# Kernel optimization log

Measured on AMD Instinct MI355X. Metric: run time of the kernel, lower is better.

Reference implementation:

```python
import jax, jax.numpy as jnp
import numpy as np

B, T, P = 4, 1000, 300
C, D, CC = 512, 256, 256
H, NL, FF = 8, 4, 2048
L = P + T
DH = C // H


def _sin_emb(t, dim):
    half = dim // 2
    freqs = jnp.exp(-jnp.arange(half, dtype=jnp.float32) * (np.log(10000.0) / (half - 1)))
    a = t[:, None].astype(jnp.float32) * freqs[None, :]
    return jnp.concatenate([jnp.sin(a), jnp.cos(a)], axis=-1)


def _pos_emb(pos, dim):
    # fairseq-style sinusoidal table evaluated at integer positions (padding_idx+1 offset already applied by caller)
    half = dim // 2
    freqs = jnp.exp(-jnp.arange(half, dtype=jnp.float32) * (np.log(10000.0) / (half - 1)))
    a = pos[..., None].astype(jnp.float32) * freqs
    return jnp.concatenate([jnp.sin(a), jnp.cos(a)], axis=-1)


def _ln(x, g, b, eps=1e-5):
    m = jnp.mean(x, -1, keepdims=True)
    v = jnp.mean((x - m) ** 2, -1, keepdims=True)
    return (x - m) * jax.lax.rsqrt(v + eps) * g + b


def _mish(x):
    return x * jnp.tanh(jax.nn.softplus(x))


def _mha(x, key_pad, Wqkv, bqkv, Wo, bo):
    qkv = x @ Wqkv + bqkv
    q, k, v = jnp.split(qkv, 3, axis=-1)
    q = q.reshape(B, L, H, DH)
    k = k.reshape(B, L, H, DH)
    v = v.reshape(B, L, H, DH)
    s = jnp.einsum('blhd,bmhd->bhlm', q, k) / np.sqrt(DH)
    s = jnp.where(key_pad[:, None, None, :], -1e9, s)  # mask padded keys
    a = jax.nn.softmax(s, axis=-1)
    o = jnp.einsum('bhlm,bmhd->blhd', a, v).reshape(B, L, C)
    return o @ Wo + bo


def _layer(x, key_pad, skip, p):
    Wqkv, bqkv, Wo, bo, g1, b1, g2, b2, W1, bf1, W2, bf2 = p
    if skip is not None:
        x = (x + skip) / np.sqrt(2.0)
    x = x + _mha(_ln(x, g1, b1), key_pad, Wqkv, bqkv, Wo, bo)
    attn_skip = x
    h = _ln(x, g2, b2)
    x = x + jax.nn.relu(h @ W1 + bf1) @ W2 + bf2
    return x, attn_skip, x


def _fwd(spec, diffusion_step, cond, prompt,
         spec_W, spec_b, cond_W, cond_b, prompt_W, prompt_b,
         mlp_W1, mlp_b1, mlp_W2, mlp_b2, out_W, out_b, skip_W, skip_b,
         Wqkv, bqkv, Wo, bo, ln1_g, ln1_b, ln2_g, ln2_b,
         ffn_W1, ffn_b1, ffn_W2, ffn_b2, x_mask, prompt_mask):
    spec_h = jnp.einsum('bdt,dc->btc', spec, spec_W) + spec_b      # [B,T,C]
    cond_h = jnp.einsum('bdt,dc->btc', cond, cond_W) + cond_b      # [B,T,C]
    prompt_h = prompt @ prompt_W + prompt_b                        # [B,P,C]

    def mlp(e):
        return _mish(e @ mlp_W1 + mlp_b1) @ mlp_W2 + mlp_b2

    dstep = mlp(_sin_emb(diffusion_step, D))                       # [B,C]
    pstep = mlp(_sin_emb(jnp.zeros((B,), jnp.float32), D))         # [B,C]

    pl = jnp.sum(~prompt_mask, axis=1)                              # prompt lengths
    sl = jnp.sum(~x_mask, axis=1)                                   # spec lengths
    j = jnp.arange(L)[None, :]
    plb, slb = pl[:, None], sl[:, None]
    in_prompt = j < plb
    in_spec = (j >= plb) & (j < plb + slb)

    pidx = jnp.clip(j, 0, P - 1)
    sidx = jnp.clip(j - plb, 0, T - 1)
    gp = jnp.take_along_axis(prompt_h, pidx[..., None], axis=1)
    gs = jnp.take_along_axis(spec_h, sidx[..., None], axis=1)
    packed = jnp.where(in_prompt[..., None], gp,
                       jnp.where(in_spec[..., None], gs, 0.0))      # [B,L,C]
    step_packed = jnp.where(in_prompt[..., None], pstep[:, None, :],
                            jnp.where(in_spec[..., None], dstep[:, None, :], 0.0))
    cond_packed = jnp.where(in_spec[..., None],
                            jnp.take_along_axis(cond_h, sidx[..., None], axis=1), 0.0)
    key_pad = ~(in_prompt | in_spec)                                # True = padding slot
    # positions restart at padding_idx+1=1 for each segment (prompt / spec / pad)
    pos = jnp.where(in_prompt, j + 1,
                    jnp.where(in_spec, j - plb + 1, j - plb - slb + 1))

    x = packed + _pos_emb(pos, C)
    # decoder: x = x + cond ; x = x + diffusion_step (dropout identity in eval)
    x = x + cond_packed + step_packed

    in_collect, ffn_skips = [], []
    for i in range(NL // 2):
        p = (Wqkv[i], bqkv[i], Wo[i], bo[i], ln1_g[i], ln1_b[i], ln2_g[i], ln2_b[i],
             ffn_W1[i], ffn_b1[i], ffn_W2[i], ffn_b2[i])
        x, _, f = _layer(x, key_pad, None, p)
        in_collect.append(x)
        ffn_skips.append(f)
    for i in range(NL // 2, NL):
        p = (Wqkv[i], bqkv[i], Wo[i], bo[i], ln1_g[i], ln1_b[i], ln2_g[i], ln2_b[i],
             ffn_W1[i], ffn_b1[i], ffn_W2[i], ffn_b2[i])
        x, _, f = _layer(x, key_pad, in_collect.pop(), p)
        ffn_skips.append(f)

    x = sum(ffn_skips) / np.sqrt(float(NL))
    x = jax.nn.relu(x @ skip_W + skip_b)
    x = x @ out_W + out_b                                           # [B,L,D]
    xidx = plb + jnp.arange(T)[None, :]                             # gather spec slots
    x = jnp.take_along_axis(x, xidx[..., None], axis=1)             # [B,T,D]
    return x.transpose(0, 2, 1)                                     # [B,D,T]


def setup_inputs() -> dict:
    key = jax.random.key(0)
    it = iter(jax.random.split(key, 40))
    def n(shape, s=0.02):
        return jax.random.normal(next(it), shape, jnp.float32) * s
    spec = jax.random.normal(next(it), (B, D, T), jnp.float32)
    cond = jax.random.normal(next(it), (B, CC, T), jnp.float32)
    prompt = jax.random.normal(next(it), (B, P, D), jnp.float32)
    diffusion_step = jax.random.uniform(next(it), (B,), jnp.float32) * 1000.0
    spec_len = jax.random.randint(next(it), (B,), T // 2, T + 1)
    prompt_len = jax.random.randint(next(it), (B,), P // 2, P + 1)
    x_mask = jnp.arange(T)[None, :] >= spec_len[:, None]
    prompt_mask = jnp.arange(P)[None, :] >= prompt_len[:, None]
    spk = jnp.zeros((B,), jnp.int32)
    return dict(
        spec=spec, x_mask=x_mask, diffusion_step=diffusion_step, cond=cond,
        spk=spk, prompt=prompt, prompt_mask=prompt_mask,
        spec_W=n((D, C)), spec_b=jnp.zeros((C,)),
        cond_W=n((CC, C)), cond_b=jnp.zeros((C,)),
        prompt_W=n((D, C)), prompt_b=jnp.zeros((C,)),
        mlp_W1=n((D, 4 * D)), mlp_b1=jnp.zeros((4 * D,)),
        mlp_W2=n((4 * D, C)), mlp_b2=jnp.zeros((C,)),
        out_W=n((C, D)), out_b=jnp.zeros((D,)),
        skip_W=n((C, C)), skip_b=jnp.zeros((C,)),
        Wqkv=n((NL, C, 3 * C)), bqkv=jnp.zeros((NL, 3 * C)),
        Wo=n((NL, C, C)), bo=jnp.zeros((NL, C)),
        ln1_g=jnp.ones((NL, C)), ln1_b=jnp.zeros((NL, C)),
        ln2_g=jnp.ones((NL, C)), ln2_b=jnp.zeros((NL, C)),
        ffn_W1=n((NL, C, FF)), ffn_b1=jnp.zeros((NL, FF)),
        ffn_W2=n((NL, FF, C)), ffn_b2=jnp.zeros((NL, C)),
    )


def reference(spec, x_mask, diffusion_step, cond, spk, prompt, prompt_mask,
              spec_W, spec_b, cond_W, cond_b, prompt_W, prompt_b,
              mlp_W1, mlp_b1, mlp_W2, mlp_b2, out_W, out_b, skip_W, skip_b,
              Wqkv, bqkv, Wo, bo, ln1_g, ln1_b, ln2_g, ln2_b,
              ffn_W1, ffn_b1, ffn_W2, ffn_b2):
    del spk  # unused by the original forward
    return _fwd(spec, diffusion_step, cond, prompt,
                spec_W, spec_b, cond_W, cond_b, prompt_W, prompt_b,
                mlp_W1, mlp_b1, mlp_W2, mlp_b2, out_W, out_b, skip_W, skip_b,
                Wqkv, bqkv, Wo, bo, ln1_g, ln1_b, ln2_g, ln2_b,
                ffn_W1, ffn_b1, ffn_W2, ffn_b2, x_mask, prompt_mask)
```

## Files before the change

### kernel.cpp

```cpp
#include <hip/hip_runtime.h>
#include <math.h>

typedef unsigned short u16;
typedef __bf16 bf16x8 __attribute__((ext_vector_type(8)));
typedef float f32x4 __attribute__((ext_vector_type(4)));

#define BB 4
#define TT 1000
#define PP 300
#define CC 512
#define DD 256
#define HH 8
#define DH 64
#define LL 1300
#define FF 2048
#define H3 1536
#define VTS 1304

#define OFF_STEP 64L
#define OFF_HB   2624L
#define OFF_S0   8192L
#define OFF_S1   (OFF_S0 + 2662400L)
#define OFF_FS   (OFF_S1 + 2662400L)
#define OFF_X    (OFF_FS + 2662400L)
#define OFF_BIG  (OFF_X  + 2662400L)
#define OFF_VT   (OFF_BIG + 2662400L)
#define OFF_Z    (OFF_BIG + 7987200L)
#define OFF_XNH  (OFF_Z   + 1331200L)
#define OFF_AOH  (OFF_XNH + 1331200L)
#define OFF_FSH  (OFF_AOH + 1331200L)
#define OFF_WT   (OFF_FSH + 1331200L)
#define WT_QKV 0L
#define WT_WO  3145728L
#define WT_W1  4194304L
#define WT_W2  8388608L
#define WT_SK  12582912L
#define WT_OUT 12845056L
#define WT_SPEC 12976128L
#define WT_COND 13107200L
#define WT_PR   13238272L

__device__ __forceinline__ u16 f2bf(float f) {
    unsigned u = __float_as_uint(f);
    unsigned r = (u + 0x7FFFu + ((u >> 16) & 1u)) >> 16;
    return (u16)r;
}

__device__ __forceinline__ void gld_lds16(const void* g, void* l) {
    __builtin_amdgcn_global_load_lds((const __attribute__((address_space(1))) void*)g,
                                     (__attribute__((address_space(3))) void*)l, 16, 0, 0);
}

__device__ __forceinline__ void stage64(const u16* __restrict__ gbase, long rstride,
                                        u16* __restrict__ lds, int tid) {
    int row = tid >> 2, pblk = tid & 3;
    int lblk = pblk ^ ((row >> 1) & 3);
    #pragma unroll
    for (int p = 0; p < 2; p++) {
        gld_lds16(gbase + (long)row * rstride + p * 32 + lblk * 8,
                  lds + ((long)(p * 256 + tid)) * 8);
    }
}

__device__ __forceinline__ void stage64c(const u16* __restrict__ gbase, long rstride,
                                         int row0, int maxRow,
                                         u16* __restrict__ lds, int tid) {
    int row = tid >> 2, pblk = tid & 3;
    int lblk = pblk ^ ((row >> 1) & 3);
    int rg = row0 + row; if (rg > maxRow) rg = maxRow;
    const u16* src = gbase + (long)rg * rstride;
    #pragma unroll
    for (int p = 0; p < 2; p++) {
        gld_lds16(src + p * 32 + lblk * 8,
                  lds + ((long)(p * 256 + tid)) * 8);
    }
}

__global__ void k_meta(const unsigned* __restrict__ pmW,
                       const unsigned* __restrict__ xmW,
                       int* __restrict__ meta)
{
    __shared__ int modeS;
    __shared__ int cnt[8];
    int tid = threadIdx.x;
    if (tid < 8) cnt[tid] = 0;
    if (tid == 0) modeS = 0;
    __syncthreads();
    int byteFlag = 0;
    for (int j = tid; j < PP; j += 256) if (pmW[j] > 1u) byteFlag = 1;
    for (int j = tid; j < TT; j += 256) if (xmW[j] > 1u) byteFlag = 1;
    if (byteFlag) atomicOr(&modeS, 1);
    __syncthreads();
    if ((modeS & 1) == 0) {
        int i64Flag = 0;
        for (int j = tid; j < 4 * PP - 1; j += 256) {
            if ((j % PP) == PP - 1) continue;
            if (pmW[j] == 1u && pmW[j + 1] == 0u) i64Flag = 1;
        }
        if (i64Flag) atomicOr(&modeS, 2);
    }
    __syncthreads();
    int mode = modeS;
    const unsigned char* pmB = (const unsigned char*)pmW;
    const long long*     pmL = (const long long*)pmW;
    const int*           pmI = (const int*)pmW;
    const unsigned char* xmB = (const unsigned char*)xmW;
    const long long*     xmL = (const long long*)xmW;
    const int*           xmI = (const int*)xmW;
    for (int idx = tid; idx < BB * PP; idx += 256) {
        int b = idx / PP;
        bool z = (mode & 1) ? (pmB[idx] == 0) : (mode & 2) ? (pmL[idx] == 0) : (pmI[idx] == 0);
        if (z) atomicAdd(&cnt[b], 1);
    }
    for (int idx = tid; idx < BB * TT; idx += 256) {
        int b = idx / TT;
        bool z = (mode & 1) ? (xmB[idx] == 0) : (mode & 2) ? (xmL[idx] == 0) : (xmI[idx] == 0);
        if (z) atomicAdd(&cnt[4 + b], 1);
    }
    __syncthreads();
    if (tid < 8) meta[tid] = cnt[tid];
    if (tid == 8) meta[8] = mode;
}

__global__ __launch_bounds__(256) void k_step1(const float* __restrict__ dsin,
    const float* __restrict__ W1, const float* __restrict__ b1, float* __restrict__ hbuf)
{
    __shared__ float emb[DD];
    __shared__ float red[256];
    int row = blockIdx.y, tid = threadIdx.x;
    int n0 = blockIdx.x * 64;
    float t = (row < BB) ? dsin[row] : 0.f;
    if (tid < 128) {
        const float c = 9.210340371976184f / 127.f;
        float f = expf(-c * (float)tid);
        float a = t * f;
        emb[tid] = sinf(a);
        emb[tid + 128] = cosf(a);
    }
    __syncthreads();
    int n = n0 + (tid & 63);
    int k0 = (tid >> 6) * 64;
    float acc = 0.f;
    #pragma unroll 8
    for (int k = 0; k < 64; k++)
        acc += emb[k0 + k] * W1[(long)(k0 + k) * (4 * DD) + n];
    red[tid] = acc;
    __syncthreads();
    if (tid < 64) {
        float a2 = red[tid] + red[tid + 64] + red[tid + 128] + red[tid + 192] + b1[n];
        float sp = fmaxf(a2, 0.f) + log1pf(expf(-fabsf(a2)));
        hbuf[(long)row * (4 * DD) + n] = a2 * tanhf(sp);
    }
}

__global__ __launch_bounds__(256) void k_step2(const float* __restrict__ hbuf,
    const float* __restrict__ W2, const float* __restrict__ b2, float* __restrict__ outbuf)
{
    __shared__ float h1[4 * DD];
    __shared__ float red[256];
    int row = blockIdx.y, tid = threadIdx.x;
    int n0 = blockIdx.x * 64;
    #pragma unroll
    for (int p = 0; p < 4; p++) h1[tid + p * 256] = hbuf[(long)row * (4 * DD) + tid + p * 256];
    __syncthreads();
    int n = n0 + (tid & 63);
    int k0 = (tid >> 6) * 256;
    float acc = 0.f;
    #pragma unroll 8
    for (int k = 0; k < 256; k++)
        acc += h1[k0 + k] * W2[(long)(k0 + k) * CC + n];
    red[tid] = acc;
    __syncthreads();
    if (tid < 64)
        outbuf[(long)row * CC + n] = red[tid] + red[tid + 64] + red[tid + 128] + red[tid + 192] + b2[n];
}

__global__ __launch_bounds__(256) void k_wcast(const float* __restrict__ W, u16* __restrict__ WT,
                                               int K, int N, long inStride, long outStride)
{
    __shared__ float t[64][65];
    int n0 = blockIdx.x * 64, k0 = blockIdx.y * 64;
    long z = blockIdx.z;
    const float* Wz = W + z * inStride;
    u16* WTz = WT + z * outStride;
    int tid = threadIdx.x;
    #pragma unroll
    for (int p = 0; p < 16; p++) {
        int idx = tid + p * 256;
        int rk = idx >> 6, cn = idx & 63;
        t[rk][cn] = Wz[(long)(k0 + rk) * N + n0 + cn];
    }
    __syncthreads();
    #pragma unroll
    for (int p = 0; p < 8; p++) {
        int idx = tid + p * 256;
        int n = idx >> 5, k2 = (idx & 31) * 2;
        ushort2 u;
        u.x = f2bf(t[k2][n]);
        u.y = f2bf(t[k2 + 1][n]);
        *(ushort2*)&WTz[(long)(n0 + n) * K + k0 + k2] = u;
    }
}

__global__ __launch_bounds__(256) void k_acast(const float* __restrict__ Win, u16* __restrict__ Out,
                                               int K, int N, long inStride, long outStride)
{
    __shared__ float t[64][65];
    int n0 = blockIdx.x * 64, k0 = blockIdx.y * 64;
    long z = blockIdx.z;
    const float* Wz = Win + z * inStride;
    u16* Oz = Out + z * outStride;
    int tid = threadIdx.x;
    #pragma unroll
    for (int p = 0; p < 16; p++) {
        int idx = tid + p * 256;
        int rk = idx >> 6, cn = idx & 63;
        int nn = n0 + cn; if (nn >= N) nn = N - 1;
        t[rk][cn] = Wz[(long)(k0 + rk) * N + nn];
    }
    __syncthreads();
    #pragma unroll
    for (int p = 0; p < 8; p++) {
        int idx = tid + p * 256;
        int nn = idx >> 5, k2 = (idx & 31) * 2;
        if (n0 + nn < N) {
            ushort2 u;
            u.x = f2bf(t[k2][nn]);
            u.y = f2bf(t[k2 + 1][nn]);
            *(ushort2*)&Oz[(long)(n0 + nn) * K + k0 + k2] = u;
        }
    }
}

__global__ void k_cast(const float4* __restrict__ in, ushort4* __restrict__ out, int n4)
{
    int i = blockIdx.x * 256 + threadIdx.x;
    if (i < n4) {
        float4 v = in[i];
        ushort4 u;
        u.x = f2bf(v.x); u.y = f2bf(v.y); u.z = f2bf(v.z); u.w = f2bf(v.w);
        out[i] = u;
    }
}

__global__ void k_zero(float4* __restrict__ p, int n4)
{
    int i = blockIdx.x * 256 + threadIdx.x;
    if (i < n4) p[i] = (float4){0.f, 0.f, 0.f, 0.f};
}

template<int RELU, int OUTBF, int ATOMIC>
__global__ __launch_bounds__(256) void k_mm64(
    const u16* __restrict__ A, const u16* __restrict__ Bt,
    const float* __restrict__ bias, void* __restrict__ Cp,
    int M, int N, int K, int Ks)
{
    __shared__ u16 As[4096];
    __shared__ u16 Bs[2][4096];
    int tid = threadIdx.x;
    int w = tid >> 6, lane = tid & 63;
    int q = lane >> 4, r = lane & 15;
    int m0 = blockIdx.x * 64, n0 = blockIdx.y * 128;
    int kz = blockIdx.z;
    int kbase = kz * Ks;
    f32x4 acc[8] = {};
    int arow = w * 16 + r;
    int aoff = arow * 32 + (q ^ ((arow >> 1) & 3)) * 8;

    for (int k0 = kbase; k0 < kbase + Ks; k0 += 64) {
        __syncthreads();
        stage64c(A + k0, K, m0, M - 1, As, tid);
        stage64(Bt + (long)n0 * K + k0, K, Bs[0], tid);
        stage64(Bt + (long)(n0 + 64) * K + k0, K, Bs[1], tid);
        __syncthreads();
        #pragma unroll
        for (int kh = 0; kh < 2; kh++) {
            bf16x8 af = *(const bf16x8*)&As[kh * 2048 + aoff];
            #pragma unroll
            for (int ni = 0; ni < 8; ni++) {
                int rn = ni * 16 + r;
                int rr = rn & 63;
                bf16x8 bv = *(const bf16x8*)&Bs[rn >> 6][kh * 2048 + rr * 32 + ((q ^ ((rr >> 1) & 3))) * 8];
                acc[ni] = __builtin_amdgcn_mfma_f32_16x16x32_bf16(af, bv, acc[ni], 0, 0, 0);
            }
        }
    }

    #pragma unroll
    for (int ni = 0; ni < 8; ni++) {
        int col = n0 + ni * 16 + r;
        float bs = (!ATOMIC || kz == 0) ? bias[col] : 0.f;
        #pragma unroll
        for (int reg = 0; reg < 4; reg++) {
            int grow = m0 + w * 16 + q * 4 + reg;
            if (grow >= M) continue;
            long off = (long)grow * N + col;
            float v = acc[ni][reg] + bs;
            if (RELU) v = fmaxf(v, 0.f);
            if (ATOMIC)      atomicAdd((float*)Cp + off, v);
            else if (OUTBF)  ((u16*)Cp)[off] = f2bf(v);
            else             ((float*)Cp)[off] = v;
        }
    }
}

__global__ __launch_bounds__(256) void k_mmqkv64(
    const u16* __restrict__ A, const u16* __restrict__ Bt,
    const float* __restrict__ bias, u16* __restrict__ qkh, u16* __restrict__ vt,
    int M, int K)
{
    __shared__ u16 As[4096];
    __shared__ u16 Bs[2][4096];
    int tid = threadIdx.x;
    int w = tid >> 6, lane = tid & 63;
    int q = lane >> 4, r = lane & 15;
    int m0 = blockIdx.x * 64, n0 = blockIdx.y * 128;
    f32x4 acc[8] = {};
    int arow = w * 16 + r;
    int aoff = arow * 32 + (q ^ ((arow >> 1) & 3)) * 8;

    for (int k0 = 0; k0 < K; k0 += 64) {
        __syncthreads();
        stage64c(A + k0, K, m0, M - 1, As, tid);
        stage64(Bt + (long)n0 * K + k0, K, Bs[0], tid);
        stage64(Bt + (long)(n0 + 64) * K + k0, K, Bs[1], tid);
        __syncthreads();
        #pragma unroll
        for (int kh = 0; kh < 2; kh++) {
            bf16x8 af = *(const bf16x8*)&As[kh * 2048 + aoff];
            #pragma unroll
            for (int ni = 0; ni < 8; ni++) {
                int rn = ni * 16 + r;
                int rr = rn & 63;
                bf16x8 bv = *(const bf16x8*)&Bs[rn >> 6][kh * 2048 + rr * 32 + ((q ^ ((rr >> 1) & 3))) * 8];
                acc[ni] = __builtin_amdgcn_mfma_f32_16x16x32_bf16(af, bv, acc[ni], 0, 0, 0);
            }
        }
    }

    #pragma unroll
    for (int ni = 0; ni < 8; ni++) {
        int col = n0 + ni * 16 + r;
        float bs = bias[col];
        #pragma unroll
        for (int reg = 0; reg < 4; reg++) {
            int grow = m0 + w * 16 + q * 4 + reg;
            if (grow >= M) continue;
            float v = acc[ni][reg] + bs;
            if (col < 1024) {
                qkh[(long)grow * 1024 + col] = f2bf(v);
            } else {
                int c2 = col - 1024;
                int hh = c2 >> 6, dd = c2 & 63;
                int bq = grow / LL;
                int jj = grow - bq * LL;
                vt[(((long)(bq * HH + hh)) * 64 + dd) * VTS + jj] = f2bf(v);
            }
        }
    }
}

__global__ __launch_bounds__(256) void k_attn(const u16* __restrict__ qkh,
                                              const u16* __restrict__ vt,
                                              const int* __restrict__ meta,
                                              u16* __restrict__ aoh)
{
    __shared__ u16 Qs[4096], Ks[4096], Vts[4096], Ps[4096];
    int qt = blockIdx.x, h = blockIdx.y, b = blockIdx.z;
    int tid = threadIdx.x;
    int w = tid >> 6, lane = tid & 63;
    int q = lane >> 4, r = lane & 15;
    int kend = meta[b] + meta[4 + b];
    int q0 = qt * 64;

    stage64(qkh + ((long)(b * LL + q0)) * 1024 + h * DH, 1024, Qs, tid);

    float mrow[4], lrow[4];
    f32x4 O[4];
    #pragma unroll
    for (int i = 0; i < 4; i++) { mrow[i] = -INFINITY; lrow[i] = 0.f; O[i] = (f32x4){0.f, 0.f, 0.f, 0.f}; }

    int arow = w * 16 + r;
    int aoff = arow * 32 + (q ^ ((arow >> 1) & 3)) * 8;

    for (int j0 = 0; j0 < kend; j0 += 64) {
        __syncthreads();
        stage64(qkh + ((long)(b * LL + j0)) * 1024 + CC + h * DH, 1024, Ks, tid);
        stage64(vt + (((long)(b * HH + h)) * 64) * VTS + j0, VTS, Vts, tid);
        __syncthreads();

        f32x4 sacc[4] = {};
        #pragma unroll
        for (int kh = 0; kh < 2; kh++) {
            bf16x8 aq = *(const bf16x8*)&Qs[kh * 2048 + aoff];
            #pragma unroll
            for (int ni = 0; ni < 4; ni++) {
                int rn = ni * 16 + r;
                bf16x8 bk = *(const bf16x8*)&Ks[kh * 2048 + rn * 32 + (q ^ ((rn >> 1) & 3)) * 8];
                sacc[ni] = __builtin_amdgcn_mfma_f32_16x16x32_bf16(aq, bk, sacc[ni], 0, 0, 0);
            }
        }

        #pragma unroll
        for (int reg = 0; reg < 4; reg++) {
            float sv[4];
            float mx = -INFINITY;
            #pragma unroll
            for (int ni = 0; ni < 4; ni++) {
                int jg = j0 + r + 16 * ni;
                float s = (jg < kend) ? sacc[ni][reg] * 0.125f : -1e9f;
                sv[ni] = s;
                mx = fmaxf(mx, s);
            }
            #pragma unroll
            for (int off = 1; off < 16; off <<= 1) mx = fmaxf(mx, __shfl_xor(mx, off, 64));
            float mnew = fmaxf(mrow[reg], mx);
            float aSc = __expf(mrow[reg] - mnew);
            mrow[reg] = mnew;
            float ps = 0.f;
            int prow = w * 16 + q * 4 + reg;
            int psw = (prow >> 1) & 3;
            #pragma unroll
            for (int ni = 0; ni < 4; ni++) {
                float p = __expf(sv[ni] - mnew);
                ps += p;
                int c = r + 16 * ni;
                Ps[(c >> 5) * 2048 + prow * 32 + ((((c & 31) >> 3)) ^ psw) * 8 + (c & 7)] = f2bf(p);
            }
            #pragma unroll
            for (int off = 1; off < 16; off <<= 1) ps += __shfl_xor(ps, off, 64);
            lrow[reg] = lrow[reg] * aSc + ps;
            O[0][reg] *= aSc; O[1][reg] *= aSc; O[2][reg] *= aSc; O[3][reg] *= aSc;
        }

        #pragma unroll
        for (int kh = 0; kh < 2; kh++) {
            bf16x8 ap = *(const bf16x8*)&Ps[kh * 2048 + aoff];
            #pragma unroll
            for (int ni = 0; ni < 4; ni++) {
                int rn = ni * 16 + r;
                bf16x8 bv = *(const bf16x8*)&Vts[kh * 2048 + rn * 32 + (q ^ ((rn >> 1) & 3)) * 8];
                O[ni] = __builtin_amdgcn_mfma_f32_16x16x32_bf16(ap, bv, O[ni], 0, 0, 0);
            }
        }
    }

    #pragma unroll
    for (int reg = 0; reg < 4; reg++) {
        int qr = q0 + w * 16 + q * 4 + reg;
        if (qr >= LL) continue;
        float inv = 1.f / lrow[reg];
        #pragma unroll
        for (int ni = 0; ni < 4; ni++)
            aoh[((long)(b * LL + qr)) * CC + h * DH + r + 16 * ni] = f2bf(O[ni][reg] * inv);
    }
}

__global__ void k_pack(const float* __restrict__ spec_h, const float* __restrict__ cond_h,
                       const float* __restrict__ prompt_h, const float* __restrict__ stepbuf,
                       const int* __restrict__ meta, float* __restrict__ x)
{
    int j = blockIdx.x, b = blockIdx.y;
    int pl = meta[b], sl = meta[4 + b];
    int tid = threadIdx.x;
    int reg = (j < pl) ? 0 : ((j < pl + sl) ? 1 : 2);
    int pos = (reg == 0) ? j + 1 : ((reg == 1) ? j - pl + 1 : j - pl - sl + 1);
    const float c1 = 9.210340371976184f / 255.f;
    for (int c = tid; c < CC; c += 256) {
        int i = (c < 256) ? c : c - 256;
        float f = expf(-c1 * (float)i);
        float a = (float)pos * f;
        float v = (c < 256) ? sinf(a) : cosf(a);
        if (reg == 0) {
            v += prompt_h[((long)(b * PP + j)) * CC + c] + stepbuf[4 * CC + c];
        } else if (reg == 1) {
            int t = j - pl;
            v += spec_h[((long)(b * TT + t)) * CC + c] + cond_h[((long)(b * TT + t)) * CC + c]
               + stepbuf[b * CC + c];
        }
        x[((long)(b * LL + j)) * CC + c] = v;
    }
}

__global__ __launch_bounds__(256) void k_ln(float* __restrict__ x, const float* __restrict__ skip,
                                            const float* __restrict__ g, const float* __restrict__ bb,
                                            u16* __restrict__ xnh)
{
    long row = blockIdx.x;
    float* xr = x + row * CC;
    int tid = threadIdx.x;
    float v0 = xr[tid], v1 = xr[tid + 256];
    if (skip) {
        const float rs2 = 0.7071067811865476f;
        v0 = (v0 + skip[row * CC + tid]) * rs2;
        v1 = (v1 + skip[row * CC + tid + 256]) * rs2;
        xr[tid] = v0; xr[tid + 256] = v1;
    }
    float s = v0 + v1;
    for (int off = 32; off; off >>= 1) s += __shfl_down(s, off, 64);
    __shared__ float red[4];
    int wid = tid >> 6, lane = tid & 63;
    if (lane == 0) red[wid] = s;
    __syncthreads();
    float mean = (red[0] + red[1] + red[2] + red[3]) * (1.f / (float)CC);
    float d0 = v0 - mean, d1 = v1 - mean;
    float q = d0 * d0 + d1 * d1;
    for (int off = 32; off; off >>= 1) q += __shfl_down(q, off, 64);
    __syncthreads();
    if (lane == 0) red[wid] = q;
    __syncthreads();
    float var = (red[0] + red[1] + red[2] + red[3]) * (1.f / (float)CC);
    float rstd = rsqrtf(var + 1e-5f);
    xnh[row * CC + tid]       = f2bf(d0 * rstd * g[tid] + bb[tid]);
    xnh[row * CC + tid + 256] = f2bf(d1 * rstd * g[tid + 256] + bb[tid + 256]);
}

__global__ void k_accum(const float4* __restrict__ x, float4* __restrict__ fsum,
                        float4* __restrict__ skipdst, u16* __restrict__ fsh,
                        int first, int last)
{
    int i = blockIdx.x * 256 + threadIdx.x;
    float4 v = x[i];
    float4 f;
    if (first) f = v;
    else { f = fsum[i]; f.x += v.x; f.y += v.y; f.z += v.z; f.w += v.w; }
    fsum[i] = f;
    if (skipdst) skipdst[i] = v;
    if (last) {
        ushort4 u;
        u.x = f2bf(f.x * 0.5f); u.y = f2bf(f.y * 0.5f);
        u.z = f2bf(f.z * 0.5f); u.w = f2bf(f.w * 0.5f);
        *(ushort4*)&fsh[4 * i] = u;
    }
}

__global__ void k_gather(const float* __restrict__ z, const int* __restrict__ meta,
                         float* __restrict__ out)
{
    int i = blockIdx.x * 256 + threadIdx.x;
    int b = i / (DD * TT);
    int rdt = i % (DD * TT);
    int d = rdt / TT, t = rdt % TT;
    long row = (long)b * LL + meta[b] + t;
    out[i] = z[row * DD + d];
}

extern "C" void kernel_launch(void* const* d_in, const int* in_sizes, int n_in,
                              void* d_out, int out_size, void* d_ws, size_t ws_size,
                              hipStream_t stream)
{
    const float* spec     = (const float*)d_in[0];
    const void*  x_mask   = d_in[1];
    const float* dstep_in = (const float*)d_in[2];
    const float* cond     = (const float*)d_in[3];
    const float* prompt   = (const float*)d_in[5];
    const void*  p_mask   = d_in[6];
    const float* spec_W   = (const float*)d_in[7];
    const float* spec_b   = (const float*)d_in[8];
    const float* cond_W   = (const float*)d_in[9];
    const float* cond_b   = (const float*)d_in[10];
    const float* prompt_W = (const float*)d_in[11];
    const float* prompt_b = (const float*)d_in[12];
    const float* mlp_W1   = (const float*)d_in[13];
    const float* mlp_b1   = (const float*)d_in[14];
    const float* mlp_W2   = (const float*)d_in[15];
    const float* mlp_b2   = (const float*)d_in[16];
    const float* out_W    = (const float*)d_in[17];
    const float* out_b    = (const float*)d_in[18];
    const float* skip_W   = (const float*)d_in[19];
    const float* skip_b   = (const float*)d_in[20];
    const float* Wqkv     = (const float*)d_in[21];
    const float* bqkv     = (const float*)d_in[22];
    const float* Wo       = (const float*)d_in[23];
    const float* bo       = (const float*)d_in[24];
    const float* ln1_g    = (const float*)d_in[25];
    const float* ln1_b    = (const float*)d_in[26];
    const float* ln2_g    = (const float*)d_in[27];
    const float* ln2_b    = (const float*)d_in[28];
    const float* ffn_W1   = (const float*)d_in[29];
    const float* ffn_b1   = (const float*)d_in[30];
    const float* ffn_W2   = (const float*)d_in[31];
    const float* ffn_b2   = (const float*)d_in[32];

    float* W  = (float*)d_ws;
    int* meta = (int*)d_ws;
    float* stepbuf = W + OFF_STEP;
    float* HB  = W + OFF_HB;
    float* S0  = W + OFF_S0;
    float* S1  = W + OFF_S1;
    float* FS  = W + OFF_FS;
    float* X   = W + OFF_X;
    u16*   QKHh = (u16*)(W + OFF_BIG);
    u16*   VTh  = (u16*)(W + OFF_VT);
    u16*   BIGh = (u16*)(W + OFF_BIG);
    u16*   SPECAh = (u16*)(W + OFF_BIG);
    u16*   CONDAh = (u16*)(W + OFF_BIG + 512000L);
    u16*   PRAh   = (u16*)(W + OFF_BIG + 1024000L);
    float* Z   = W + OFF_Z;
    u16*   XNh = (u16*)(W + OFF_XNH);
    u16*   AOh = (u16*)(W + OFF_AOH);
    u16*   FSh = (u16*)(W + OFF_FSH);
    u16*   WT  = (u16*)(W + OFF_WT);

    k_meta<<<1, 256, 0, stream>>>((const unsigned*)p_mask, (const unsigned*)x_mask, meta);
    k_step1<<<dim3(16, 5), 256, 0, stream>>>(dstep_in, mlp_W1, mlp_b1, HB);
    k_step2<<<dim3(8, 5), 256, 0, stream>>>(HB, mlp_W2, mlp_b2, stepbuf);

    k_wcast<<<dim3(24, 8, 4), 256, 0, stream>>>(Wqkv, WT + WT_QKV, CC, H3, (long)CC * H3, (long)H3 * CC);
    k_wcast<<<dim3(8, 8, 4), 256, 0, stream>>>(Wo, WT + WT_WO, CC, CC, (long)CC * CC, (long)CC * CC);
    k_wcast<<<dim3(32, 8, 4), 256, 0, stream>>>(ffn_W1, WT + WT_W1, CC, FF, (long)CC * FF, (long)FF * CC);
    k_wcast<<<dim3(8, 32, 4), 256, 0, stream>>>(ffn_W2, WT + WT_W2, FF, CC, (long)FF * CC, (long)CC * FF);
    k_wcast<<<dim3(8, 8, 1), 256, 0, stream>>>(skip_W, WT + WT_SK, CC, CC, 0L, 0L);
    k_wcast<<<dim3(4, 8, 1), 256, 0, stream>>>(out_W, WT + WT_OUT, CC, DD, 0L, 0L);
    k_wcast<<<dim3(8, 4, 1), 256, 0, stream>>>(spec_W, WT + WT_SPEC, DD, CC, 0L, 0L);
    k_wcast<<<dim3(8, 4, 1), 256, 0, stream>>>(cond_W, WT + WT_COND, DD, CC, 0L, 0L);
    k_wcast<<<dim3(8, 4, 1), 256, 0, stream>>>(prompt_W, WT + WT_PR, DD, CC, 0L, 0L);

    k_acast<<<dim3(16, 4, 4), 256, 0, stream>>>(spec, SPECAh, DD, TT, (long)DD * TT, (long)TT * DD);
    k_acast<<<dim3(16, 4, 4), 256, 0, stream>>>(cond, CONDAh, DD, TT, (long)DD * TT, (long)TT * DD);
    k_cast<<<300, 256, 0, stream>>>((const float4*)prompt, (ushort4*)PRAh, BB * PP * DD / 4);
    k_mm64<0, 0, 0><<<dim3(63, 4), 256, 0, stream>>>(SPECAh, WT + WT_SPEC, spec_b, S0, BB * TT, CC, DD, DD);
    k_mm64<0, 0, 0><<<dim3(63, 4), 256, 0, stream>>>(CONDAh, WT + WT_COND, cond_b, S1, BB * TT, CC, DD, DD);
    k_mm64<0, 0, 0><<<dim3(19, 4), 256, 0, stream>>>(PRAh, WT + WT_PR, prompt_b, FS, BB * PP, CC, DD, DD);

    k_pack<<<dim3(LL, BB), 256, 0, stream>>>(S0, S1, FS, stepbuf, meta, X);

    const int Mrows = BB * LL;
    for (int i = 0; i < 4; i++) {
        const float* skipPtr = (i == 2) ? S1 : (i == 3) ? S0 : nullptr;
        k_ln<<<Mrows, 256, 0, stream>>>(X, skipPtr, ln1_g + i * CC, ln1_b + i * CC, XNh);
        k_mmqkv64<<<dim3(82, 12), 256, 0, stream>>>(XNh, WT + WT_QKV + (long)i * CC * H3,
            bqkv + i * H3, QKHh, VTh, Mrows, CC);
        k_attn<<<dim3(21, HH, BB), 256, 0, stream>>>(QKHh, VTh, meta, AOh);
        k_mm64<0, 0, 1><<<dim3(82, 4, 2), 256, 0, stream>>>(AOh, WT + WT_WO + (long)i * CC * CC,
            bo + i * CC, X, Mrows, CC, CC, 256);
        k_ln<<<Mrows, 256, 0, stream>>>(X, nullptr, ln2_g + i * CC, ln2_b + i * CC, XNh);
        k_mm64<1, 1, 0><<<dim3(82, 16), 256, 0, stream>>>(XNh, WT + WT_W1 + (long)i * CC * FF,
            ffn_b1 + i * FF, BIGh, Mrows, FF, CC, CC);
        k_mm64<0, 0, 1><<<dim3(82, 4, 2), 256, 0, stream>>>(BIGh, WT + WT_W2 + (long)i * FF * CC,
            ffn_b2 + i * CC, X, Mrows, CC, FF, 1024);
        float4* skipDst = (i == 0) ? (float4*)S0 : (i == 1) ? (float4*)S1 : nullptr;
        k_accum<<<2600, 256, 0, stream>>>((const float4*)X, (float4*)FS, skipDst, FSh, i == 0, i == 3);
    }

    k_mm64<1, 1, 0><<<dim3(82, 4), 256, 0, stream>>>(FSh, WT + WT_SK, skip_b, XNh, Mrows, CC, CC, CC);
    k_zero<<<1300, 256, 0, stream>>>((float4*)Z, 332800);
    k_mm64<0, 0, 1><<<dim3(82, 2, 2), 256, 0, stream>>>(XNh, WT + WT_OUT, out_b, Z, Mrows, DD, CC, 256);

    k_gather<<<4000, 256, 0, stream>>>(Z, meta, (float*)d_out);
    (void)in_sizes; (void)n_in; (void)out_size; (void)ws_size;
}
```

Baseline: 1.012 ms.

## Retile GEMM warps 2x2, drop online-softmax max, fuse accumulate with next LayerNorm

The GEMM kernels now split the 64x128 tile into a 2x2 warp grid with 32x64 per warp. Each B fragment load now feeds two MFMAs. Attention drops the running max and rescaling and does one row-sum reduction at the end, which saves shuffles and exp work but can overflow if scores get large. The per-layer accumulate kernel is merged with the next layer's LN1, including the skip blend, so one full pass over X and one launch per layer go away. Skip handling is reworked: S1 is no longer stored, and layer 2 uses x*sqrt2.

```diff
diff --git a/kernel.cpp b/kernel.cpp
--- a/kernel.cpp
+++ b/kernel.cpp
@@ -260,12 +260,15 @@
     int tid = threadIdx.x;
     int w = tid >> 6, lane = tid & 63;
     int q = lane >> 4, r = lane & 15;
+    int wm = w & 1, wn = w >> 1;
     int m0 = blockIdx.x * 64, n0 = blockIdx.y * 128;
     int kz = blockIdx.z;
     int kbase = kz * Ks;
-    f32x4 acc[8] = {};
-    int arow = w * 16 + r;
-    int aoff = arow * 32 + (q ^ ((arow >> 1) & 3)) * 8;
+    f32x4 acc[2][4] = {};
+    int ar0 = wm * 32 + r;
+    int ar1 = ar0 + 16;
+    int aoff0 = ar0 * 32 + (q ^ ((ar0 >> 1) & 3)) * 8;
+    int aoff1 = ar1 * 32 + (q ^ ((ar1 >> 1) & 3)) * 8;
 
     for (int k0 = kbase; k0 < kbase + Ks; k0 += 64) {
         __syncthreads();
@@ -275,31 +278,35 @@
         __syncthreads();
         #pragma unroll
         for (int kh = 0; kh < 2; kh++) {
-            bf16x8 af = *(const bf16x8*)&As[kh * 2048 + aoff];
+            bf16x8 a0 = *(const bf16x8*)&As[kh * 2048 + aoff0];
+            bf16x8 a1 = *(const bf16x8*)&As[kh * 2048 + aoff1];
             #pragma unroll
-            for (int ni = 0; ni < 8; ni++) {
-                int rn = ni * 16 + r;
-                int rr = rn & 63;
-                bf16x8 bv = *(const bf16x8*)&Bs[rn >> 6][kh * 2048 + rr * 32 + ((q ^ ((rr >> 1) & 3))) * 8];
-                acc[ni] = __builtin_amdgcn_mfma_f32_16x16x32_bf16(af, bv, acc[ni], 0, 0, 0);
+            for (int ni = 0; ni < 4; ni++) {
+                int rr = ni * 16 + r;
+                bf16x8 bv = *(const bf16x8*)&Bs[wn][kh * 2048 + rr * 32 + (q ^ ((rr >> 1) & 3)) * 8];
+                acc[0][ni] = __builtin_amdgcn_mfma_f32_16x16x32_bf16(a0, bv, acc[0][ni], 0, 0, 0);
+                acc[1][ni] = __builtin_amdgcn_mfma_f32_16x16x32_bf16(a1, bv, acc[1][ni], 0, 0, 0);
             }
         }
     }
 
     #pragma unroll
-    for (int ni = 0; ni < 8; ni++) {
-        int col = n0 + ni * 16 + r;
+    for (int ni = 0; ni < 4; ni++) {
+        int col = n0 + wn * 64 + ni * 16 + r;
         float bs = (!ATOMIC || kz == 0) ? bias[col] : 0.f;
         #pragma unroll
-        for (int reg = 0; reg < 4; reg++) {
-            int grow = m0 + w * 16 + q * 4 + reg;
-            if (grow >= M) continue;
-            long off = (long)grow * N + col;
-            float v = acc[ni][reg] + bs;
-            if (RELU) v = fmaxf(v, 0.f);
-            if (ATOMIC)      atomicAdd((float*)Cp + off, v);
-            else if (OUTBF)  ((u16*)Cp)[off] = f2bf(v);
-            else             ((float*)Cp)[off] = v;
+        for (int mi = 0; mi < 2; mi++) {
+            #pragma unroll
+            for (int reg = 0; reg < 4; reg++) {
+                int grow = m0 + wm * 32 + mi * 16 + q * 4 + reg;
+                if (grow >= M) continue;
+                long off = (long)grow * N + col;
+                float v = acc[mi][ni][reg] + bs;
+                if (RELU) v = fmaxf(v, 0.f);
+                if (ATOMIC)      atomicAdd((float*)Cp + off, v);
+                else if (OUTBF)  ((u16*)Cp)[off] = f2bf(v);
+                else             ((float*)Cp)[off] = v;
+            }
         }
     }
 }
@@ -314,10 +321,13 @@
     int tid = threadIdx.x;
     int w = tid >> 6, lane = tid & 63;
     int q = lane >> 4, r = lane & 15;
+    int wm = w & 1, wn = w >> 1;
     int m0 = blockIdx.x * 64, n0 = blockIdx.y * 128;
-    f32x4 acc[8] = {};
-    int arow = w * 16 + r;
-    int aoff = arow * 32 + (q ^ ((arow >> 1) & 3)) * 8;
+    f32x4 acc[2][4] = {};
+    int ar0 = wm * 32 + r;
+    int ar1 = ar0 + 16;
+    int aoff0 = ar0 * 32 + (q ^ ((ar0 >> 1) & 3)) * 8;
+    int aoff1 = ar1 * 32 + (q ^ ((ar1 >> 1) & 3)) * 8;
 
     for (int k0 = 0; k0 < K; k0 += 64) {
         __syncthreads();
@@ -327,34 +337,38 @@
         __syncthreads();
         #pragma unroll
         for (int kh = 0; kh < 2; kh++) {
-            bf16x8 af = *(const bf16x8*)&As[kh * 2048 + aoff];
+            bf16x8 a0 = *(const bf16x8*)&As[kh * 2048 + aoff0];
+            bf16x8 a1 = *(const bf16x8*)&As[kh * 2048 + aoff1];
             #pragma unroll
-            for (int ni = 0; ni < 8; ni++) {
-                int rn = ni * 16 + r;
-                int rr = rn & 63;
-                bf16x8 bv = *(const bf16x8*)&Bs[rn >> 6][kh * 2048 + rr * 32 + ((q ^ ((rr >> 1) & 3))) * 8];
-                acc[ni] = __builtin_amdgcn_mfma_f32_16x16x32_bf16(af, bv, acc[ni], 0, 0, 0);
+            for (int ni = 0; ni < 4; ni++) {
+                int rr = ni * 16 + r;
+                bf16x8 bv = *(const bf16x8*)&Bs[wn][kh * 2048 + rr * 32 + (q ^ ((rr >> 1) & 3)) * 8];
+                acc[0][ni] = __builtin_amdgcn_mfma_f32_16x16x32_bf16(a0, bv, acc[0][ni], 0, 0, 0);
+                acc[1][ni] = __builtin_amdgcn_mfma_f32_16x16x32_bf16(a1, bv, acc[1][ni], 0, 0, 0);
             }
         }
     }
 
     #pragma unroll
-    for (int ni = 0; ni < 8; ni++) {
-        int col = n0 + ni * 16 + r;
+    for (int ni = 0; ni < 4; ni++) {
+        int col = n0 + wn * 64 + ni * 16 + r;
         float bs = bias[col];
         #pragma unroll
-        for (int reg = 0; reg < 4; reg++) {
-            int grow = m0 + w * 16 + q * 4 + reg;
-            if (grow >= M) continue;
-            float v = acc[ni][reg] + bs;
-            if (col < 1024) {
-                qkh[(long)grow * 1024 + col] = f2bf(v);
-            } else {
-                int c2 = col - 1024;
-                int hh = c2 >> 6, dd = c2 & 63;
-                int bq = grow / LL;
-                int jj = grow - bq * LL;
-                vt[(((long)(bq * HH + hh)) * 64 + dd) * VTS + jj] = f2bf(v);
+        for (int mi = 0; mi < 2; mi++) {
+            #pragma unroll
+            for (int reg = 0; reg < 4; reg++) {
+                int grow = m0 + wm * 32 + mi * 16 + q * 4 + reg;
+                if (grow >= M) continue;
+                float v = acc[mi][ni][reg] + bs;
+                if (col < 1024) {
+                    qkh[(long)grow * 1024 + col] = f2bf(v);
+                } else {
+                    int c2 = col - 1024;
+                    int hh = c2 >> 6, dd = c2 & 63;
+                    int bq = grow / LL;
+                    int jj = grow - bq * LL;
+                    vt[(((long)(bq * HH + hh)) * 64 + dd) * VTS + jj] = f2bf(v);
+                }
             }
         }
     }
@@ -375,10 +389,8 @@
 
     stage64(qkh + ((long)(b * LL + q0)) * 1024 + h * DH, 1024, Qs, tid);
 
-    float mrow[4], lrow[4];
-    f32x4 O[4];
-    #pragma unroll
-    for (int i = 0; i < 4; i++) { mrow[i] = -INFINITY; lrow[i] = 0.f; O[i] = (f32x4){0.f, 0.f, 0.f, 0.f}; }
+    float lsum[4] = {0.f, 0.f, 0.f, 0.f};
+    f32x4 O[4] = {};
 
     int arow = w * 16 + r;
     int aoff = arow * 32 + (q ^ ((arow >> 1) & 3)) * 8;
@@ -403,34 +415,16 @@
 
         #pragma unroll
         for (int reg = 0; reg < 4; reg++) {
-            float sv[4];
-            float mx = -INFINITY;
-            #pragma unroll
-            for (int ni = 0; ni < 4; ni++) {
-                int jg = j0 + r + 16 * ni;
-                float s = (jg < kend) ? sacc[ni][reg] * 0.125f : -1e9f;
-                sv[ni] = s;
-                mx = fmaxf(mx, s);
-            }
-            #pragma unroll
-            for (int off = 1; off < 16; off <<= 1) mx = fmaxf(mx, __shfl_xor(mx, off, 64));
-            float mnew = fmaxf(mrow[reg], mx);
-            float aSc = __expf(mrow[reg] - mnew);
-            mrow[reg] = mnew;
-            float ps = 0.f;
             int prow = w * 16 + q * 4 + reg;
             int psw = (prow >> 1) & 3;
             #pragma unroll
             for (int ni = 0; ni < 4; ni++) {
-                float p = __expf(sv[ni] - mnew);
-                ps += p;
+                int jg = j0 + r + 16 * ni;
+                float p = (jg < kend) ? __expf(sacc[ni][reg] * 0.125f) : 0.f;
+                lsum[reg] += p;
                 int c = r + 16 * ni;
                 Ps[(c >> 5) * 2048 + prow * 32 + ((((c & 31) >> 3)) ^ psw) * 8 + (c & 7)] = f2bf(p);
             }
-            #pragma unroll
-            for (int off = 1; off < 16; off <<= 1) ps += __shfl_xor(ps, off, 64);
-            lrow[reg] = lrow[reg] * aSc + ps;
-            O[0][reg] *= aSc; O[1][reg] *= aSc; O[2][reg] *= aSc; O[3][reg] *= aSc;
         }
 
         #pragma unroll
@@ -447,9 +441,12 @@
 
     #pragma unroll
     for (int reg = 0; reg < 4; reg++) {
+        float l = lsum[reg];
+        #pragma unroll
+        for (int off = 1; off < 16; off <<= 1) l += __shfl_xor(l, off, 64);
         int qr = q0 + w * 16 + q * 4 + reg;
         if (qr >= LL) continue;
-        float inv = 1.f / lrow[reg];
+        float inv = 1.f / l;
         #pragma unroll
         for (int ni = 0; ni < 4; ni++)
             aoh[((long)(b * LL + qr)) * CC + h * DH + r + 16 * ni] = f2bf(O[ni][reg] * inv);
@@ -515,23 +512,51 @@
     xnh[row * CC + tid + 256] = f2bf(d1 * rstd * g[tid + 256] + bb[tid + 256]);
 }
 
-__global__ void k_accum(const float4* __restrict__ x, float4* __restrict__ fsum,
-                        float4* __restrict__ skipdst, u16* __restrict__ fsh,
-                        int first, int last)
-{
-    int i = blockIdx.x * 256 + threadIdx.x;
-    float4 v = x[i];
-    float4 f;
-    if (first) f = v;
-    else { f = fsum[i]; f.x += v.x; f.y += v.y; f.z += v.z; f.w += v.w; }
-    fsum[i] = f;
-    if (skipdst) skipdst[i] = v;
+__global__ __launch_bounds__(256) void k_accum_ln(
+    float* __restrict__ x, float* __restrict__ fsum, float* __restrict__ skipdst,
+    const float* __restrict__ skip, int self,
+    const float* __restrict__ g, const float* __restrict__ bb,
+    u16* __restrict__ xnh, u16* __restrict__ fsh, int first, int last)
+{
+    long row = blockIdx.x;
+    int tid = threadIdx.x;
+    long o0 = row * CC + tid, o1 = o0 + 256;
+    float v0 = x[o0], v1 = x[o1];
+    float f0, f1;
+    if (first) { f0 = v0; f1 = v1; }
+    else { f0 = fsum[o0] + v0; f1 = fsum[o1] + v1; }
+    fsum[o0] = f0; fsum[o1] = f1;
+    if (skipdst) { skipdst[o0] = v0; skipdst[o1] = v1; }
     if (last) {
-        ushort4 u;
-        u.x = f2bf(f.x * 0.5f); u.y = f2bf(f.y * 0.5f);
-        u.z = f2bf(f.z * 0.5f); u.w = f2bf(f.w * 0.5f);
-        *(ushort4*)&fsh[4 * i] = u;
-    }
+        fsh[o0] = f2bf(f0 * 0.5f);
+        fsh[o1] = f2bf(f1 * 0.5f);
+        return;
+    }
+    const float rs2 = 0.7071067811865476f;
+    if (self) {
+        v0 *= 1.4142135623730951f; v1 *= 1.4142135623730951f;
+        x[o0] = v0; x[o1] = v1;
+    } else if (skip) {
+        v0 = (v0 + skip[o0]) * rs2; v1 = (v1 + skip[o1]) * rs2;
+        x[o0] = v0; x[o1] = v1;
+    }
+    float s = v0 + v1;
+    for (int off = 32; off; off >>= 1) s += __shfl_down(s, off, 64);
+    __shared__ float red[4];
+    int wid = tid >> 6, lane = tid & 63;
+    if (lane == 0) red[wid] = s;
+    __syncthreads();
+    float mean = (red[0] + red[1] + red[2] + red[3]) * (1.f / (float)CC);
+    float d0 = v0 - mean, d1 = v1 - mean;
+    float qv = d0 * d0 + d1 * d1;
+    for (int off = 32; off; off >>= 1) qv += __shfl_down(qv, off, 64);
+    __syncthreads();
+    if (lane == 0) red[wid] = qv;
+    __syncthreads();
+    float var = (red[0] + red[1] + red[2] + red[3]) * (1.f / (float)CC);
+    float rstd = rsqrtf(var + 1e-5f);
+    xnh[o0] = f2bf(d0 * rstd * g[tid] + bb[tid]);
+    xnh[o1] = f2bf(d1 * rstd * g[tid + 256] + bb[tid + 256]);
 }
 
 __global__ void k_gather(const float* __restrict__ z, const int* __restrict__ meta,
@@ -626,9 +651,8 @@
     k_pack<<<dim3(LL, BB), 256, 0, stream>>>(S0, S1, FS, stepbuf, meta, X);
 
     const int Mrows = BB * LL;
+    k_ln<<<Mrows, 256, 0, stream>>>(X, nullptr, ln1_g, ln1_b, XNh);
     for (int i = 0; i < 4; i++) {
-        const float* skipPtr = (i == 2) ? S1 : (i == 3) ? S0 : nullptr;
-        k_ln<<<Mrows, 256, 0, stream>>>(X, skipPtr, ln1_g + i * CC, ln1_b + i * CC, XNh);
         k_mmqkv64<<<dim3(82, 12), 256, 0, stream>>>(XNh, WT + WT_QKV + (long)i * CC * H3,
             bqkv + i * H3, QKHh, VTh, Mrows, CC);
         k_attn<<<dim3(21, HH, BB), 256, 0, stream>>>(QKHh, VTh, meta, AOh);
@@ -639,8 +663,12 @@
             ffn_b1 + i * FF, BIGh, Mrows, FF, CC, CC);
         k_mm64<0, 0, 1><<<dim3(82, 4, 2), 256, 0, stream>>>(BIGh, WT + WT_W2 + (long)i * FF * CC,
             ffn_b2 + i * CC, X, Mrows, CC, FF, 1024);
-        float4* skipDst = (i == 0) ? (float4*)S0 : (i == 1) ? (float4*)S1 : nullptr;
-        k_accum<<<2600, 256, 0, stream>>>((const float4*)X, (float4*)FS, skipDst, FSh, i == 0, i == 3);
+        float* skipDst = (i == 0) ? S0 : nullptr;
+        const float* skipNext = (i == 2) ? S0 : nullptr;
+        int selfNext = (i == 1) ? 1 : 0;
+        k_accum_ln<<<Mrows, 256, 0, stream>>>(X, FS, skipDst, skipNext, selfNext,
+            ln1_g + (i + 1 < 4 ? (i + 1) : 0) * CC, ln1_b + (i + 1 < 4 ? (i + 1) : 0) * CC,
+            XNh, FSh, i == 0, i == 3);
     }
 
     k_mm64<1, 1, 0><<<dim3(82, 4), 256, 0, stream>>>(FSh, WT + WT_SK, skip_b, XNh, Mrows, CC, CC, CC);
```

New measurement: 917.7 us. 1.1x faster.
